# Optimization experiments

Measured on AMD Instinct MI355X. Metric: run time of the kernel, lower is better.

The kernel has to match this reference:

```python
import jax, jax.numpy as jnp
import numpy as np

K = 16  # kNN neighbors
R = 4   # upsampling ratio


def knn_idx(x, k):
    """Per-cloud kNN (self excluded). x: [B,N,C] -> idx [B,N,k] int32."""
    sq = jnp.sum(x * x, axis=-1)  # [B,N]
    d = sq[:, :, None] + sq[:, None, :] - 2.0 * jnp.einsum('bnc,bmc->bnm', x, x)
    n = x.shape[1]
    d = d + jnp.eye(n, dtype=x.dtype) * jnp.asarray(1e9, x.dtype)  # exclude self-loop
    _, idx = jax.lax.top_k(-d, k)  # k smallest distances
    return idx


def edge_conv(x, idx, W, b):
    """EdgeConv: mlp([x_i, x_j - x_i]) with max aggregation over neighbors.
    x: [B,N,C], idx: [B,N,k] -> [B,N,out]."""
    nbr = jax.vmap(lambda xb, ib: xb[ib])(x, idx)            # [B,N,k,C] gather
    ctr = jnp.broadcast_to(x[:, :, None, :], nbr.shape)
    e = jnp.concatenate([ctr, nbr - ctr], axis=-1)           # [B,N,k,2C]
    h = jax.nn.relu(jnp.einsum('bnkc,cd->bnkd', e, W) + b)
    return jnp.max(h, axis=2)                                # max aggregate


def setup_inputs() -> dict:
    key = jax.random.key(0)
    ks = jax.random.split(key, 16)
    B, N = 8, 2048
    chans = [3, 32, 32, 64]  # DynConv stack: 3->32->32->64
    C = chans[-1]

    def lin(k, fan_in, fan_out):
        s = 1.0 / np.sqrt(fan_in)
        return jax.random.uniform(k, (fan_in, fan_out), jnp.float32, -s, s)

    inp = {'x': jax.random.normal(ks[0], (B, N, 3), jnp.float32)}
    # DynConv (EdgeConv) weights: Linear(2*in, out)
    for i in range(3):
        inp[f'W{i}'] = lin(ks[1 + i], 2 * chans[i], chans[i + 1])
        inp[f'b{i}'] = jnp.zeros((chans[i + 1],), jnp.float32)
    # NodeShuffle: EdgeConv(C -> R*C) then shuffle N -> N*R
    inp['Wup'] = lin(ks[5], 2 * C, R * C)
    inp['bup'] = jnp.zeros((R * C,), jnp.float32)
    # Reconstructor MLP([64,128,64,3])
    rdims = [64, 128, 64, 3]
    for i in range(3):
        inp[f'Wr{i}'] = lin(ks[6 + i], rdims[i], rdims[i + 1])
        inp[f'br{i}'] = jnp.zeros((rdims[i + 1],), jnp.float32)
    return inp


def reference(x, W0, b0, W1, b1, W2, b2, Wup, bup, Wr0, br0, Wr1, br1, Wr2, br2):
    # Dynamic feature extractor: recompute kNN on current feature space each layer
    for W, b in ((W0, b0), (W1, b1), (W2, b2)):
        idx = knn_idx(x, K)
        x = edge_conv(x, idx, W, b)
    # NodeShuffle upsampler: EdgeConv to R*C channels, then shuffle nodes
    idx = knn_idx(x, K)
    h = edge_conv(x, idx, Wup, bup)              # [B,N,R*C]
    B, N, _ = h.shape
    C = h.shape[-1] // R
    x = h.reshape(B, N, R, C).reshape(B, N * R, C)  # [B,N*R,C]
    # Reconstructor MLP -> xyz
    x = jax.nn.relu(x @ Wr0 + br0)
    x = jax.nn.relu(x @ Wr1 + br1)
    return x @ Wr2 + br2                          # [B,N*R,3]
```

## Files before the change

kernel.cpp:

```cpp
#include <hip/hip_runtime.h>

#define B_ 8
#define N_ 2048
#define K_ 16
#define M_ (B_*N_)

typedef unsigned long long ull;

__device__ __forceinline__ ull kmin(ull a, ull b) { return a < b ? a : b; }

template<int C>
__global__ __launch_bounds__(256, 2) void knn2_kernel(const float* __restrict__ X,
                                                      int* __restrict__ idx_out) {
    constexpr int TJ = 128;
    constexpr int SJ = TJ + 4;
    constexpr int SS = TJ + 4;
    constexpr int SI = 36;
    __shared__ float xiT[C][SI];
    __shared__ float xjT[C][SJ];
    __shared__ float S[32][SS];

    int tid = threadIdx.x;
    int sb = (blockIdx.x & 7) * (M_ / 32 / 8) + (blockIdx.x >> 3);
    int m0 = sb * 32;
    int b  = m0 >> 11;
    int i0 = m0 & (N_ - 1);
    const float* Xb = X + ((size_t)b << 11) * C;

    if constexpr (C == 3) {
        if (tid < 96) { int ir = tid / 3, c = tid - ir * 3;
            xiT[c][ir] = X[(size_t)(m0 + ir) * 3 + c]; }
    } else {
        constexpr int C4 = C / 4;
        for (int e4 = tid; e4 < 32 * C4; e4 += 256) {
            int ir = e4 / C4, c4 = e4 - ir * C4;
            float4 v = *(const float4*)&X[(size_t)(m0 + ir) * C + c4 * 4];
            xiT[c4*4+0][ir] = v.x; xiT[c4*4+1][ir] = v.y;
            xiT[c4*4+2][ir] = v.z; xiT[c4*4+3][ir] = v.w;
        }
    }

    ull t[16];
#pragma unroll
    for (int q = 0; q < 16; ++q) t[q] = ~0ull;
    float t15f = __uint_as_float(0x7FFFFFFFu);

    int ig = tid >> 5, jl4 = tid & 31;
    int irow = tid >> 3, r = tid & 7;
    int i_loc = i0 + irow;

    for (int jt = 0; jt < N_ / TJ; ++jt) {
        __syncthreads();
        if constexpr (C == 3) {
            for (int e = tid; e < TJ * 3; e += 256) {
                int jl = e / 3, c = e - jl * 3;
                xjT[c][jl] = Xb[(size_t)jt * TJ * 3 + e];
            }
        } else {
            constexpr int C4 = C / 4;
            for (int e4 = tid; e4 < 32 * C4; e4 += 256) {
                int jb = e4 / C4, c4 = e4 - jb * C4;
                const float* src = &Xb[(size_t)(jt * TJ + jb * 4) * C + c4 * 4];
                float4 v0 = *(const float4*)&src[0];
                float4 v1 = *(const float4*)&src[C];
                float4 v2 = *(const float4*)&src[2 * C];
                float4 v3 = *(const float4*)&src[3 * C];
                *(float4*)&xjT[c4*4+0][jb*4] = make_float4(v0.x, v1.x, v2.x, v3.x);
                *(float4*)&xjT[c4*4+1][jb*4] = make_float4(v0.y, v1.y, v2.y, v3.y);
                *(float4*)&xjT[c4*4+2][jb*4] = make_float4(v0.z, v1.z, v2.z, v3.z);
                *(float4*)&xjT[c4*4+3][jb*4] = make_float4(v0.w, v1.w, v2.w, v3.w);
            }
        }
        __syncthreads();

        float acc[4][4];
#pragma unroll
        for (int u = 0; u < 4; ++u) {
            acc[u][0] = 0.f; acc[u][1] = 0.f; acc[u][2] = 0.f; acc[u][3] = 0.f;
        }
#pragma unroll 4
        for (int c = 0; c < C; ++c) {
            float4 xi4 = *(const float4*)&xiT[c][ig * 4];
            float4 xj4 = *(const float4*)&xjT[c][jl4 * 4];
            float xiv[4] = {xi4.x, xi4.y, xi4.z, xi4.w};
            float xjv[4] = {xj4.x, xj4.y, xj4.z, xj4.w};
#pragma unroll
            for (int u = 0; u < 4; ++u)
#pragma unroll
                for (int v = 0; v < 4; ++v) {
                    float df = xiv[u] - xjv[v];
                    acc[u][v] = fmaf(df, df, acc[u][v]);
                }
        }
#pragma unroll
        for (int u = 0; u < 4; ++u)
            *(float4*)&S[ig * 4 + u][jl4 * 4] =
                make_float4(acc[u][0], acc[u][1], acc[u][2], acc[u][3]);
        __syncthreads();

        int jbase = jt * TJ + r * 16;
#pragma unroll
        for (int w = 0; w < 4; ++w) {
            float4 sv = *(const float4*)&S[irow][r * 16 + w * 4];
            float se[4] = {sv.x, sv.y, sv.z, sv.w};
            float mn = fminf(fminf(se[0], se[1]), fminf(se[2], se[3]));
            if (!(mn > t15f)) {
#pragma unroll
                for (int e = 0; e < 4; ++e) {
                    float s = se[e];
                    if (!(s > t15f)) {
                        int jg = jbase + w * 4 + e;
                        if (jg != i_loc) {
                            unsigned uu = __float_as_uint(s) ^ 0x80000000u;
                            ull key = ((ull)uu << 32) | (unsigned)jg;
                            if (key < t[15]) {
                                t[15] = key;
#pragma unroll
                                for (int s2 = 15; s2 > 0; --s2) {
                                    ull a = t[s2 - 1], bb2 = t[s2];
                                    bool sw = bb2 < a;
                                    t[s2 - 1] = sw ? bb2 : a;
                                    t[s2]     = sw ? a : bb2;
                                }
                                t15f = __uint_as_float((unsigned)(t[15] >> 32) ^ 0x80000000u);
                            }
                        }
                    }
                }
            }
        }
    }

#pragma unroll
    for (int msk = 1; msk <= 4; msk <<= 1) {
        ull o[16];
#pragma unroll
        for (int q = 0; q < 16; ++q)
            o[q] = __shfl_xor((ull)t[q], msk, 64);
        ull nt[16];
#pragma unroll
        for (int q = 0; q < 16; ++q) nt[q] = kmin(t[q], o[15 - q]);
#pragma unroll
        for (int s2 = 8; s2 >= 1; s2 >>= 1) {
#pragma unroll
            for (int q = 0; q < 16; ++q) {
                if (!(q & s2)) {
                    ull a = nt[q], bb2 = nt[q | s2];
                    bool sw = bb2 < a;
                    nt[q]      = sw ? bb2 : a;
                    nt[q | s2] = sw ? a : bb2;
                }
            }
        }
#pragma unroll
        for (int q = 0; q < 16; ++q) t[q] = nt[q];
    }

    if (r == 0) {
        int* op = idx_out + (size_t)(m0 + irow) * K_;
#pragma unroll
        for (int q = 0; q < 16; ++q) op[q] = (int)(unsigned)(t[q] & 0xffffffffull);
    }
}

template<int C>
__global__ __launch_bounds__(256) void proj_kernel(const float* __restrict__ X,
        const float* __restrict__ W, double* __restrict__ T1NB,
        int Dfull, int DH, int doff) {
    __shared__ float XsT[C][68];
    __shared__ float Bs[C][64];
    int tid = threadIdx.x;
    int m0 = blockIdx.x * 64;
    int n0 = blockIdx.y * 64;

    if constexpr (C == 3) {
        if (tid < 192) { int row = tid / 3, c = tid - row * 3;
            XsT[c][row] = X[(size_t)(m0 + row) * 3 + c]; }
    } else {
        constexpr int C4 = C / 4;
        for (int e4 = tid; e4 < 64 * C4; e4 += 256) {
            int row = e4 / C4, c4 = e4 - row * C4;
            float4 v = *(const float4*)&X[(size_t)(m0 + row) * C + c4 * 4];
            XsT[c4*4+0][row] = v.x; XsT[c4*4+1][row] = v.y;
            XsT[c4*4+2][row] = v.z; XsT[c4*4+3][row] = v.w;
        }
    }
    for (int e = tid; e < C * 64; e += 256) {
        int c = e >> 6, dc = e & 63;
        int n = n0 + dc;
        float wv = (n < DH) ? W[(size_t)c * Dfull + doff + n]
                            : W[(size_t)(C + c) * Dfull + doff + (n - DH)];
        Bs[c][dc] = wv;
    }
    __syncthreads();

    int tx = tid & 15, ty = tid >> 4;
    double acc[4][4];
#pragma unroll
    for (int u = 0; u < 4; ++u) { acc[u][0]=0.0; acc[u][1]=0.0; acc[u][2]=0.0; acc[u][3]=0.0; }

#pragma unroll 4
    for (int c = 0; c < C; ++c) {
        float4 xv = *(const float4*)&XsT[c][ty * 4];
        float4 wv = *(const float4*)&Bs[c][tx * 4];
        double xd[4] = {(double)xv.x, (double)xv.y, (double)xv.z, (double)xv.w};
        double wd[4] = {(double)wv.x, (double)wv.y, (double)wv.z, (double)wv.w};
#pragma unroll
        for (int u = 0; u < 4; ++u)
#pragma unroll
            for (int v = 0; v < 4; ++v)
                acc[u][v] = fma(xd[u], wd[v], acc[u][v]);
    }
#pragma unroll
    for (int u = 0; u < 4; ++u) {
        double* dst = &T1NB[(size_t)(m0 + ty * 4 + u) * (2 * DH) + n0 + tx * 4];
        *(double2*)&dst[0] = make_double2(acc[u][0], acc[u][1]);
        *(double2*)&dst[2] = make_double2(acc[u][2], acc[u][3]);
    }
}

template<int DH>
__global__ __launch_bounds__(256) void gmax_kernel(const double* __restrict__ T1NB,
        const int* __restrict__ idx, const float* __restrict__ bias,
        float* __restrict__ O, int Dfull, int doff) {
    constexpr int TPP = DH / 2;
    constexpr int PPB = 256 / TPP;
    __shared__ int idxs[PPB * 16];

    int tid = threadIdx.x;
    int cpx = gridDim.x >> 3;
    int sb = ((int)blockIdx.x & 7) * cpx + ((int)blockIdx.x >> 3);
    int m0 = sb * PPB;

    if (tid < PPB * 16)
        idxs[tid] = idx[(size_t)(m0 + tid / 16) * K_ + (tid & 15)];
    __syncthreads();

    int p = tid / TPP, dh = tid % TPP;
    int d0 = dh * 2;
    int m = m0 + p;
    int b = m >> 11;
    size_t base = (size_t)m * (2 * DH);
    double2 t1  = *(const double2*)&T1NB[base + d0];
    double2 nbi = *(const double2*)&T1NB[base + DH + d0];
    double ba = t1.x - nbi.x, bb = t1.y - nbi.y;
    double ma = -1.0e300, mb = -1.0e300;
    size_t rowb = ((size_t)(b << 11)) * (2 * DH) + DH + d0;
    const int* ip = &idxs[p * 16];
#pragma unroll 4
    for (int k = 0; k < 16; ++k) {
        int j = ip[k];
        double2 q = *(const double2*)&T1NB[rowb + (size_t)j * (2 * DH)];
        ma = fmax(ma, ba + q.x);
        mb = fmax(mb, bb + q.y);
    }
    float2 o;
    o.x = (float)fmax(ma + (double)bias[doff + d0],     0.0);
    o.y = (float)fmax(mb + (double)bias[doff + d0 + 1], 0.0);
    *(float2*)&O[(size_t)m * Dfull + doff + d0] = o;
}

__global__ __launch_bounds__(256) void recon_kernel(const float* __restrict__ U,
        const float* __restrict__ W0, const float* __restrict__ b0,
        const float* __restrict__ W1, const float* __restrict__ b1,
        const float* __restrict__ W2, const float* __restrict__ b2,
        float* __restrict__ O) {
    __shared__ float F[32 * 68];
    __shared__ float H1[128 * 33];
    __shared__ float H2[64 * 33];
    __shared__ float W2s[64 * 4];
    __shared__ float b0s[128], b1s[64], b2s[4];

    int tid = threadIdx.x;
    int m0 = blockIdx.x * 32;

    {
        const float4* src = (const float4*)(U + (size_t)m0 * 64);
        for (int e4 = tid; e4 < 32 * 16; e4 += 256) {
            int p = e4 >> 4, c4 = e4 & 15;
            *(float4*)&F[p * 68 + c4 * 4] = src[e4];
        }
    }
    if (tid < 192) W2s[(tid / 3) * 4 + (tid % 3)] = W2[tid];
    if (tid < 128) b0s[tid] = b0[tid];
    else if (tid < 192) b1s[tid - 128] = b1[tid - 128];
    else if (tid == 192) { b2s[0] = b2[0]; b2s[1] = b2[1]; b2s[2] = b2[2]; }
    __syncthreads();

    int p = tid >> 3, s = tid & 7;

    float acc[16];
#pragma unroll
    for (int q = 0; q < 16; ++q) acc[q] = 0.f;
    for (int c = 0; c < 64; ++c) {
        float a = F[p * 68 + c];
#pragma unroll
        for (int q = 0; q < 4; ++q) {
            float4 w = *(const float4*)&W0[c * 128 + s * 4 + q * 32];
            acc[q * 4 + 0] = fmaf(a, w.x, acc[q * 4 + 0]);
            acc[q * 4 + 1] = fmaf(a, w.y, acc[q * 4 + 1]);
            acc[q * 4 + 2] = fmaf(a, w.z, acc[q * 4 + 2]);
            acc[q * 4 + 3] = fmaf(a, w.w, acc[q * 4 + 3]);
        }
    }
#pragma unroll
    for (int q = 0; q < 4; ++q)
#pragma unroll
        for (int i2 = 0; i2 < 4; ++i2) {
            int dd = s * 4 + q * 32 + i2;
            H1[dd * 33 + p] = fmaxf(acc[q * 4 + i2] + b0s[dd], 0.f);
        }
    __syncthreads();

    float a2[8];
#pragma unroll
    for (int q = 0; q < 8; ++q) a2[q] = 0.f;
    for (int c = 0; c < 128; ++c) {
        float a = H1[c * 33 + p];
#pragma unroll
        for (int q = 0; q < 2; ++q) {
            float4 w = *(const float4*)&W1[c * 64 + s * 4 + q * 32];
            a2[q * 4 + 0] = fmaf(a, w.x, a2[q * 4 + 0]);
            a2[q * 4 + 1] = fmaf(a, w.y, a2[q * 4 + 1]);
            a2[q * 4 + 2] = fmaf(a, w.z, a2[q * 4 + 2]);
            a2[q * 4 + 3] = fmaf(a, w.w, a2[q * 4 + 3]);
        }
    }
#pragma unroll
    for (int q = 0; q < 2; ++q)
#pragma unroll
        for (int i2 = 0; i2 < 4; ++i2) {
            int dd = s * 4 + q * 32 + i2;
            H2[dd * 33 + p] = fmaxf(a2[q * 4 + i2] + b1s[dd], 0.f);
        }
    __syncthreads();

    if (tid < 96) {
        int p3 = tid / 3, d3 = tid - p3 * 3;
        float av = 0.f;
#pragma unroll
        for (int c = 0; c < 64; ++c)
            av = fmaf(H2[c * 33 + p3], W2s[c * 4 + d3], av);
        O[(size_t)(m0 + p3) * 3 + d3] = av + b2s[d3];
    }
}

extern "C" void kernel_launch(void* const* d_in, const int* in_sizes, int n_in,
                              void* d_out, int out_size, void* d_ws, size_t ws_size,
                              hipStream_t stream) {
    const float* x   = (const float*)d_in[0];
    const float* W0  = (const float*)d_in[1];
    const float* b0  = (const float*)d_in[2];
    const float* W1  = (const float*)d_in[3];
    const float* b1  = (const float*)d_in[4];
    const float* W2  = (const float*)d_in[5];
    const float* b2  = (const float*)d_in[6];
    const float* Wup = (const float*)d_in[7];
    const float* bup = (const float*)d_in[8];
    const float* Wr0 = (const float*)d_in[9];
    const float* br0 = (const float*)d_in[10];
    const float* Wr1 = (const float*)d_in[11];
    const float* br1 = (const float*)d_in[12];
    const float* Wr2 = (const float*)d_in[13];
    const float* br2 = (const float*)d_in[14];
    float* out = (float*)d_out;

    char* ws = (char*)d_ws;
    size_t o = 0;
    auto alloc = [&](size_t nbytes) {
        void* pp = ws + o;
        o += (nbytes + 255) & ~(size_t)255;
        return pp;
    };
    float*  X1   = (float*)alloc((size_t)M_ * 32 * 4);
    float*  X2   = (float*)alloc((size_t)M_ * 32 * 4);
    float*  X3   = (float*)alloc((size_t)M_ * 64 * 4);
    float*  H    = (float*)alloc((size_t)M_ * 256 * 4);
    int*    idxb = (int*)alloc((size_t)M_ * 16 * 4);
    double* T1NB = (double*)alloc((size_t)M_ * 256 * 8);

    knn2_kernel<3><<<512, 256, 0, stream>>>(x, idxb);
    proj_kernel<3><<<dim3(M_ / 64, 1), 256, 0, stream>>>(x, W0, T1NB, 32, 32, 0);
    gmax_kernel<32><<<M_ / 16, 256, 0, stream>>>(T1NB, idxb, b0, X1, 32, 0);
    knn2_kernel<32><<<512, 256, 0, stream>>>(X1, idxb);
    proj_kernel<32><<<dim3(M_ / 64, 1), 256, 0, stream>>>(X1, W1, T1NB, 32, 32, 0);
    gmax_kernel<32><<<M_ / 16, 256, 0, stream>>>(T1NB, idxb, b1, X2, 32, 0);
    knn2_kernel<32><<<512, 256, 0, stream>>>(X2, idxb);
    proj_kernel<32><<<dim3(M_ / 64, 2), 256, 0, stream>>>(X2, W2, T1NB, 64, 64, 0);
    gmax_kernel<64><<<M_ / 8, 256, 0, stream>>>(T1NB, idxb, b2, X3, 64, 0);
    knn2_kernel<64><<<512, 256, 0, stream>>>(X3, idxb);
    proj_kernel<64><<<dim3(M_ / 64, 4), 256, 0, stream>>>(X3, Wup, T1NB, 256, 128, 0);
    gmax_kernel<128><<<M_ / 4, 256, 0, stream>>>(T1NB, idxb, bup, H, 256, 0);
    proj_kernel<64><<<dim3(M_ / 64, 4), 256, 0, stream>>>(X3, Wup, T1NB, 256, 128, 128);
    gmax_kernel<128><<<M_ / 4, 256, 0, stream>>>(T1NB, idxb, bup, H, 256, 128);
    recon_kernel<<<2048, 256, 0, stream>>>(H, Wr0, br0, Wr1, br1, Wr2, br2, out);
}
```

Baseline: 1.115 ms.

## Pre-transpose features for kNN loads and use fp32 buffers in upsampler EdgeConv

Adds a transpose kernel that writes features channel-major per cloud, so the kNN kernel can fill its shared tiles with plain float4 row loads instead of gathering and transposing in registers. The shared score-tile stride and per-thread column mapping change to interleave columns and reduce bank conflicts. The final upsampling EdgeConv stores its projections and runs the max reduction in fp32 instead of fp64, which halves that buffer's traffic. This costs four extra transpose launches and some precision in the last layer, where near-tie neighbour maxima could round differently.

```diff
diff --git a/kernel.cpp b/kernel.cpp
--- a/kernel.cpp
+++ b/kernel.cpp
@@ -8,15 +8,26 @@
 typedef unsigned long long ull;
 
 __device__ __forceinline__ ull kmin(ull a, ull b) { return a < b ? a : b; }
+__device__ __forceinline__ float  fmx(float a, float b)  { return fmaxf(a, b); }
+__device__ __forceinline__ double fmx(double a, double b){ return fmax(a, b); }
+
+__global__ __launch_bounds__(256) void transpose_kernel(const float* __restrict__ X,
+                                                        float* __restrict__ XT, int C) {
+    int t = blockIdx.x * 256 + threadIdx.x;
+    if (t >= M_ * C) return;
+    int c = t >> 14;
+    int m = t & (M_ - 1);
+    int b = m >> 11, n = m & (N_ - 1);
+    XT[((size_t)b * C + c) * N_ + n] = X[(size_t)m * C + c];
+}
 
 template<int C>
-__global__ __launch_bounds__(256, 2) void knn2_kernel(const float* __restrict__ X,
+__global__ __launch_bounds__(256, 2) void knnD_kernel(const float* __restrict__ XT,
                                                       int* __restrict__ idx_out) {
     constexpr int TJ = 128;
     constexpr int SJ = TJ + 4;
-    constexpr int SS = TJ + 4;
-    constexpr int SI = 36;
-    __shared__ float xiT[C][SI];
+    constexpr int SS = TJ + 12;
+    __shared__ float xiT[C][36];
     __shared__ float xjT[C][SJ];
     __shared__ float S[32][SS];
 
@@ -25,19 +36,11 @@
     int m0 = sb * 32;
     int b  = m0 >> 11;
     int i0 = m0 & (N_ - 1);
-    const float* Xb = X + ((size_t)b << 11) * C;
-
-    if constexpr (C == 3) {
-        if (tid < 96) { int ir = tid / 3, c = tid - ir * 3;
-            xiT[c][ir] = X[(size_t)(m0 + ir) * 3 + c]; }
-    } else {
-        constexpr int C4 = C / 4;
-        for (int e4 = tid; e4 < 32 * C4; e4 += 256) {
-            int ir = e4 / C4, c4 = e4 - ir * C4;
-            float4 v = *(const float4*)&X[(size_t)(m0 + ir) * C + c4 * 4];
-            xiT[c4*4+0][ir] = v.x; xiT[c4*4+1][ir] = v.y;
-            xiT[c4*4+2][ir] = v.z; xiT[c4*4+3][ir] = v.w;
-        }
+    const float* XTb = XT + (size_t)b * C * N_;
+
+    for (int e4 = tid; e4 < C * 8; e4 += 256) {
+        int c = e4 >> 3, ch = e4 & 7;
+        *(float4*)&xiT[c][ch * 4] = *(const float4*)&XTb[(size_t)c * N_ + i0 + ch * 4];
     }
 
     ull t[16];
@@ -51,25 +54,10 @@
 
     for (int jt = 0; jt < N_ / TJ; ++jt) {
         __syncthreads();
-        if constexpr (C == 3) {
-            for (int e = tid; e < TJ * 3; e += 256) {
-                int jl = e / 3, c = e - jl * 3;
-                xjT[c][jl] = Xb[(size_t)jt * TJ * 3 + e];
-            }
-        } else {
-            constexpr int C4 = C / 4;
-            for (int e4 = tid; e4 < 32 * C4; e4 += 256) {
-                int jb = e4 / C4, c4 = e4 - jb * C4;
-                const float* src = &Xb[(size_t)(jt * TJ + jb * 4) * C + c4 * 4];
-                float4 v0 = *(const float4*)&src[0];
-                float4 v1 = *(const float4*)&src[C];
-                float4 v2 = *(const float4*)&src[2 * C];
-                float4 v3 = *(const float4*)&src[3 * C];
-                *(float4*)&xjT[c4*4+0][jb*4] = make_float4(v0.x, v1.x, v2.x, v3.x);
-                *(float4*)&xjT[c4*4+1][jb*4] = make_float4(v0.y, v1.y, v2.y, v3.y);
-                *(float4*)&xjT[c4*4+2][jb*4] = make_float4(v0.z, v1.z, v2.z, v3.z);
-                *(float4*)&xjT[c4*4+3][jb*4] = make_float4(v0.w, v1.w, v2.w, v3.w);
-            }
+        for (int e4 = tid; e4 < C * 32; e4 += 256) {
+            int c = e4 >> 5, ch = e4 & 31;
+            *(float4*)&xjT[c][ch * 4] =
+                *(const float4*)&XTb[(size_t)c * N_ + jt * TJ + ch * 4];
         }
         __syncthreads();
 
@@ -98,18 +86,18 @@
                 make_float4(acc[u][0], acc[u][1], acc[u][2], acc[u][3]);
         __syncthreads();
 
-        int jbase = jt * TJ + r * 16;
 #pragma unroll
         for (int w = 0; w < 4; ++w) {
-            float4 sv = *(const float4*)&S[irow][r * 16 + w * 4];
+            float4 sv = *(const float4*)&S[irow][r * 4 + 32 * w];
             float se[4] = {sv.x, sv.y, sv.z, sv.w};
             float mn = fminf(fminf(se[0], se[1]), fminf(se[2], se[3]));
             if (!(mn > t15f)) {
+                int jbase = jt * TJ + r * 4 + 32 * w;
 #pragma unroll
                 for (int e = 0; e < 4; ++e) {
                     float s = se[e];
                     if (!(s > t15f)) {
-                        int jg = jbase + w * 4 + e;
+                        int jg = jbase + e;
                         if (jg != i_loc) {
                             unsigned uu = __float_as_uint(s) ^ 0x80000000u;
                             ull key = ((ull)uu << 32) | (unsigned)jg;
@@ -163,9 +151,9 @@
     }
 }
 
-template<int C>
+template<int C, typename TO>
 __global__ __launch_bounds__(256) void proj_kernel(const float* __restrict__ X,
-        const float* __restrict__ W, double* __restrict__ T1NB,
+        const float* __restrict__ W, TO* __restrict__ T1NB,
         int Dfull, int DH, int doff) {
     __shared__ float XsT[C][68];
     __shared__ float Bs[C][64];
@@ -213,14 +201,19 @@
     }
 #pragma unroll
     for (int u = 0; u < 4; ++u) {
-        double* dst = &T1NB[(size_t)(m0 + ty * 4 + u) * (2 * DH) + n0 + tx * 4];
-        *(double2*)&dst[0] = make_double2(acc[u][0], acc[u][1]);
-        *(double2*)&dst[2] = make_double2(acc[u][2], acc[u][3]);
-    }
-}
-
-template<int DH>
-__global__ __launch_bounds__(256) void gmax_kernel(const double* __restrict__ T1NB,
+        TO* dst = &T1NB[(size_t)(m0 + ty * 4 + u) * (2 * DH) + n0 + tx * 4];
+        if constexpr (sizeof(TO) == 8) {
+            *(double2*)&dst[0] = make_double2(acc[u][0], acc[u][1]);
+            *(double2*)&dst[2] = make_double2(acc[u][2], acc[u][3]);
+        } else {
+            *(float4*)&dst[0] = make_float4((float)acc[u][0], (float)acc[u][1],
+                                            (float)acc[u][2], (float)acc[u][3]);
+        }
+    }
+}
+
+template<int DH, typename TE>
+__global__ __launch_bounds__(256) void gmax_kernel(const TE* __restrict__ T1NB,
         const int* __restrict__ idx, const float* __restrict__ bias,
         float* __restrict__ O, int Dfull, int doff) {
     constexpr int TPP = DH / 2;
@@ -241,22 +234,23 @@
     int m = m0 + p;
     int b = m >> 11;
     size_t base = (size_t)m * (2 * DH);
-    double2 t1  = *(const double2*)&T1NB[base + d0];
-    double2 nbi = *(const double2*)&T1NB[base + DH + d0];
-    double ba = t1.x - nbi.x, bb = t1.y - nbi.y;
-    double ma = -1.0e300, mb = -1.0e300;
+    TE t1a = T1NB[base + d0],      t1b = T1NB[base + d0 + 1];
+    TE nba = T1NB[base + DH + d0], nbb = T1NB[base + DH + d0 + 1];
+    TE ba = t1a - nba, bb2 = t1b - nbb;
+    TE ma = (TE)-1.0e30, mb = (TE)-1.0e30;
     size_t rowb = ((size_t)(b << 11)) * (2 * DH) + DH + d0;
     const int* ip = &idxs[p * 16];
 #pragma unroll 4
     for (int k = 0; k < 16; ++k) {
         int j = ip[k];
-        double2 q = *(const double2*)&T1NB[rowb + (size_t)j * (2 * DH)];
-        ma = fmax(ma, ba + q.x);
-        mb = fmax(mb, bb + q.y);
+        TE qa = T1NB[rowb + (size_t)j * (2 * DH)];
+        TE qb = T1NB[rowb + (size_t)j * (2 * DH) + 1];
+        ma = fmx(ma, ba + qa);
+        mb = fmx(mb, bb2 + qb);
     }
     float2 o;
-    o.x = (float)fmax(ma + (double)bias[doff + d0],     0.0);
-    o.y = (float)fmax(mb + (double)bias[doff + d0 + 1], 0.0);
+    o.x = (float)fmx(ma + (TE)bias[doff + d0],     (TE)0);
+    o.y = (float)fmx(mb + (TE)bias[doff + d0 + 1], (TE)0);
     *(float2*)&O[(size_t)m * Dfull + doff + d0] = o;
 }
 
@@ -372,26 +366,32 @@
         o += (nbytes + 255) & ~(size_t)255;
         return pp;
     };
-    float*  X1   = (float*)alloc((size_t)M_ * 32 * 4);
-    float*  X2   = (float*)alloc((size_t)M_ * 32 * 4);
-    float*  X3   = (float*)alloc((size_t)M_ * 64 * 4);
-    float*  H    = (float*)alloc((size_t)M_ * 256 * 4);
-    int*    idxb = (int*)alloc((size_t)M_ * 16 * 4);
-    double* T1NB = (double*)alloc((size_t)M_ * 256 * 8);
-
-    knn2_kernel<3><<<512, 256, 0, stream>>>(x, idxb);
-    proj_kernel<3><<<dim3(M_ / 64, 1), 256, 0, stream>>>(x, W0, T1NB, 32, 32, 0);
-    gmax_kernel<32><<<M_ / 16, 256, 0, stream>>>(T1NB, idxb, b0, X1, 32, 0);
-    knn2_kernel<32><<<512, 256, 0, stream>>>(X1, idxb);
-    proj_kernel<32><<<dim3(M_ / 64, 1), 256, 0, stream>>>(X1, W1, T1NB, 32, 32, 0);
-    gmax_kernel<32><<<M_ / 16, 256, 0, stream>>>(T1NB, idxb, b1, X2, 32, 0);
-    knn2_kernel<32><<<512, 256, 0, stream>>>(X2, idxb);
-    proj_kernel<32><<<dim3(M_ / 64, 2), 256, 0, stream>>>(X2, W2, T1NB, 64, 64, 0);
-    gmax_kernel<64><<<M_ / 8, 256, 0, stream>>>(T1NB, idxb, b2, X3, 64, 0);
-    knn2_kernel<64><<<512, 256, 0, stream>>>(X3, idxb);
-    proj_kernel<64><<<dim3(M_ / 64, 4), 256, 0, stream>>>(X3, Wup, T1NB, 256, 128, 0);
-    gmax_kernel<128><<<M_ / 4, 256, 0, stream>>>(T1NB, idxb, bup, H, 256, 0);
-    proj_kernel<64><<<dim3(M_ / 64, 4), 256, 0, stream>>>(X3, Wup, T1NB, 256, 128, 128);
-    gmax_kernel<128><<<M_ / 4, 256, 0, stream>>>(T1NB, idxb, bup, H, 256, 128);
+    float*  X1    = (float*)alloc((size_t)M_ * 32 * 4);
+    float*  X2    = (float*)alloc((size_t)M_ * 32 * 4);
+    float*  X3    = (float*)alloc((size_t)M_ * 64 * 4);
+    float*  H     = (float*)alloc((size_t)M_ * 256 * 4);
+    int*    idxb  = (int*)alloc((size_t)M_ * 16 * 4);
+    double* T1NBd = (double*)alloc((size_t)M_ * 128 * 8);
+    float*  T1NBf = (float*)alloc((size_t)M_ * 256 * 4);
+    float*  XT    = (float*)alloc((size_t)M_ * 64 * 4);
+
+    transpose_kernel<<<(M_ * 3) / 256, 256, 0, stream>>>(x, XT, 3);
+    knnD_kernel<3><<<512, 256, 0, stream>>>(XT, idxb);
+    proj_kernel<3, double><<<dim3(M_ / 64, 1), 256, 0, stream>>>(x, W0, T1NBd, 32, 32, 0);
+    gmax_kernel<32, double><<<M_ / 16, 256, 0, stream>>>(T1NBd, idxb, b0, X1, 32, 0);
+    transpose_kernel<<<(M_ * 32) / 256, 256, 0, stream>>>(X1, XT, 32);
+    knnD_kernel<32><<<512, 256, 0, stream>>>(XT, idxb);
+    proj_kernel<32, double><<<dim3(M_ / 64, 1), 256, 0, stream>>>(X1, W1, T1NBd, 32, 32, 0);
+    gmax_kernel<32, double><<<M_ / 16, 256, 0, stream>>>(T1NBd, idxb, b1, X2, 32, 0);
+    transpose_kernel<<<(M_ * 32) / 256, 256, 0, stream>>>(X2, XT, 32);
+    knnD_kernel<32><<<512, 256, 0, stream>>>(XT, idxb);
+    proj_kernel<32, double><<<dim3(M_ / 64, 2), 256, 0, stream>>>(X2, W2, T1NBd, 64, 64, 0);
+    gmax_kernel<64, double><<<M_ / 8, 256, 0, stream>>>(T1NBd, idxb, b2, X3, 64, 0);
+    transpose_kernel<<<(M_ * 64) / 256, 256, 0, stream>>>(X3, XT, 64);
+    knnD_kernel<64><<<512, 256, 0, stream>>>(XT, idxb);
+    proj_kernel<64, float><<<dim3(M_ / 64, 4), 256, 0, stream>>>(X3, Wup, T1NBf, 256, 128, 0);
+    gmax_kernel<128, float><<<M_ / 4, 256, 0, stream>>>(T1NBf, idxb, bup, H, 256, 0);
+    proj_kernel<64, float><<<dim3(M_ / 64, 4), 256, 0, stream>>>(X3, Wup, T1NBf, 256, 128, 128);
+    gmax_kernel<128, float><<<M_ / 4, 256, 0, stream>>>(T1NBf, idxb, bup, H, 256, 128);
     recon_kernel<<<2048, 256, 0, stream>>>(H, Wr0, br0, Wr1, br1, Wr2, br2, out);
 }
```

After: 1.150 ms. +3.1%, slower.
